# Performance work log

Hardware: AMD Instinct MI355X
Metric: run time of the kernel (lower is better)

Reference implementation:

```python
import jax, jax.numpy as jnp
import numpy as np

B, L, HID, H = 2, 384, 512, 8
D = HID // H  # head_dim = 64


def setup_inputs() -> dict:
    key = jax.random.key(0)
    ks = jax.random.split(key, 16)
    s = 0.02
    return {
        "query": jax.random.normal(ks[0], (B, L, HID), jnp.float32),
        "key_": jax.random.normal(ks[1], (B, L, HID), jnp.float32),
        "value": jax.random.normal(ks[2], (B, L, HID), jnp.float32),
        "mask": jnp.ones((B, 1, 1, L), jnp.int32),
        # fc_q/k/v/o: nn.Linear(hid_dim, hid_dim)
        "Wq": jax.random.normal(ks[3], (HID, HID), jnp.float32) * s,
        "bq": jnp.zeros((HID,), jnp.float32),
        "Wk": jax.random.normal(ks[4], (HID, HID), jnp.float32) * s,
        "bk": jnp.zeros((HID,), jnp.float32),
        "Wv": jax.random.normal(ks[5], (HID, HID), jnp.float32) * s,
        "bv": jnp.zeros((HID,), jnp.float32),
        "Wo": jax.random.normal(ks[6], (HID, HID), jnp.float32) * s,
        "bo": jnp.zeros((HID,), jnp.float32),
        # additive-attention score MLP: W1, W2: Linear(D, D); v: Linear(D, 1)
        "W1": jax.random.normal(ks[7], (D, D), jnp.float32) * s,
        "b1": jnp.zeros((D,), jnp.float32),
        "W2": jax.random.normal(ks[8], (D, D), jnp.float32) * s,
        "b2": jnp.zeros((D,), jnp.float32),
        "vw": jax.random.normal(ks[9], (1, D), jnp.float32) * s,
        "vb": jnp.zeros((1,), jnp.float32),
    }


def reference(query, key_, value, mask, Wq, bq, Wk, bk, Wv, bv, Wo, bo,
              W1, b1, W2, b2, vw, vb):
    b = query.shape[0]
    # projections (torch Linear: x @ W.T + b)
    Q = query @ Wq.T + bq
    K = key_ @ Wk.T + bk
    V = value @ Wv.T + bv
    # [b, h, l, d]
    def split_heads(x):
        return x.reshape(b, -1, H, D).transpose(0, 2, 1, 3)
    Q, K, V = split_heads(Q), split_heads(K), split_heads(V)
    # additive (Bahdanau-style) score: v^T tanh(W1 q + W2 k)
    tQ = Q @ W1.T + b1            # [b, h, lq, d]
    tK = K @ W2.T + b2            # [b, h, lk, d]
    e = jnp.tanh(tQ[:, :, :, None, :] + tK[:, :, None, :, :])  # [b,h,lq,lk,d]
    energy = jnp.einsum('bhqkd,d->bhqk', e, vw[0]) + vb[0]      # [b,h,lq,lk]
    energy = jnp.where(mask == 0, jnp.float32(-1e10), energy)
    attention = jax.nn.softmax(energy, axis=-1)
    x = jnp.einsum('bhqk,bhkd->bhqd', attention, V)  # dropout p=0 (eval)
    x = x.transpose(0, 2, 1, 3).reshape(b, -1, HID)
    x = x @ Wo.T + bo
    return x, attention
```

## Files before the change

kernel.cpp:

```cpp
#include <hip/hip_runtime.h>

#define BATCH 2
#define LSEQ 384
#define NHID 512
#define NH 8
#define DH 64
#define BH (BATCH*NH)
#define XELEMS ((size_t)768 * NHID)
#define TQ 8
#define QTILES (LSEQ/TQ)

typedef unsigned short ushort_t;
typedef __attribute__((ext_vector_type(8))) short bf16x8;
typedef __attribute__((ext_vector_type(4))) float f32x4;

__device__ __forceinline__ float bf2f(ushort_t u) {
    unsigned int v = ((unsigned int)u) << 16;
    return __uint_as_float(v);
}
__device__ __forceinline__ ushort_t f2bf(float f) {
    unsigned int u = __float_as_uint(f);
    unsigned int lsb = (u >> 16) & 1u;
    u += 0x7fffu + lsb;
    return (ushort_t)(u >> 16);
}
__device__ __forceinline__ float ld1(const void* p, size_t i, int f) {
    return f ? ((const float*)p)[i] : bf2f(((const ushort_t*)p)[i]);
}
__device__ __forceinline__ float4 ld4(const void* p, size_t i, int f) {
    if (f) return ((const float4*)p)[i >> 2];
    ushort4 u = ((const ushort4*)p)[i >> 2];
    return make_float4(bf2f(u.x), bf2f(u.y), bf2f(u.z), bf2f(u.w));
}
__device__ __forceinline__ int block_detect(const unsigned int* q, int* cnt) {
    int t = threadIdx.x;
    if (t == 0) *cnt = 0;
    __syncthreads();
    int n = blockDim.x < 256 ? blockDim.x : 256;
    if (t < n) {
        unsigned int elo = (q[t] >> 7) & 0xFFu;
        if (elo >= 100u && elo <= 150u) atomicAdd(cnt, 1);
    }
    __syncthreads();
    return (*cnt * 2 > n) ? 0 : 1;
}
__device__ __forceinline__ uint4 packu4(float4 a, float4 b) {
    uint4 r;
    r.x = (unsigned)f2bf(a.x) | ((unsigned)f2bf(a.y) << 16);
    r.y = (unsigned)f2bf(a.z) | ((unsigned)f2bf(a.w) << 16);
    r.z = (unsigned)f2bf(b.x) | ((unsigned)f2bf(b.y) << 16);
    r.w = (unsigned)f2bf(b.z) | ((unsigned)f2bf(b.w) << 16);
    return r;
}
__device__ __forceinline__ bf16x8 pack_bf8(float4 a, float4 b) {
    bf16x8 r;
    r[0] = (short)f2bf(a.x); r[1] = (short)f2bf(a.y);
    r[2] = (short)f2bf(a.z); r[3] = (short)f2bf(a.w);
    r[4] = (short)f2bf(b.x); r[5] = (short)f2bf(b.y);
    r[6] = (short)f2bf(b.z); r[7] = (short)f2bf(b.w);
    return r;
}

#define OFF_P     16
#define PSTRIDE   393216
#define OFF_BQE   2359312
#define OFF_BKE   2359824
#define OFF_ETQ   2360336
#define OFF_ETKT  2753552
#define OFF_VH    3146768
#define OFF_XH    3539984

#define LDSTR 72

__global__ __launch_bounds__(128) void gemm_qkv(
    const void* qp, const void* kp, const void* vp,
    const void* Wqp, const void* Wkp, const void* Wvp,
    const void* W1p, const void* W2p,
    const void* bqp, const void* bkp, const void* b1p, const void* b2p,
    float* __restrict__ ws)
{
    __shared__ int s_cnt;
    __shared__ ushort_t smA[32 * LDSTR];
    __shared__ ushort_t smB[64 * LDSTR];
    const int f = block_detect((const unsigned int*)qp, &s_cnt);

    const int z = blockIdx.z;
    const int mode = z >> 1, ks = z & 1;
    const int kbase = ks * 256;
    const void* A = (mode == 0) ? qp : (mode == 1) ? kp : vp;
    const void* W = (mode == 0) ? Wqp : (mode == 1) ? Wkp : Wvp;
    const void* W1x = (mode == 1) ? W2p : W1p;
    float* P = ws + OFF_P + (size_t)z * PSTRIDE;

    const int h    = blockIdx.x;
    const int col0 = h * 64;
    const int row0 = blockIdx.y * 32;
    const int t = threadIdx.x;
    const int w = t >> 6, l16 = t & 15, quad = (t & 63) >> 4;

    const int arow = t >> 2, acol = (t & 3) * 16;
    const int brow = t >> 1, bcol = (t & 1) * 32;
    const size_t abase = (size_t)(row0 + arow) * 512 + kbase + acol;
    const size_t bbase = (size_t)(col0 + brow) * 512 + kbase + bcol;

    float4 a4[4], b4[8];
    #pragma unroll
    for (int i = 0; i < 4; i++) a4[i] = ld4(A, abase + i * 4, f);
    #pragma unroll
    for (int i = 0; i < 8; i++) b4[i] = ld4(W, bbase + i * 4, f);

    f32x4 acc[4];
    #pragma unroll
    for (int nt = 0; nt < 4; nt++) acc[nt] = (f32x4){0.f, 0.f, 0.f, 0.f};

    for (int k0 = 0; k0 < 256; k0 += 64) {
        __syncthreads();
        *reinterpret_cast<uint4*>(&smA[arow * LDSTR + acol])     = packu4(a4[0], a4[1]);
        *reinterpret_cast<uint4*>(&smA[arow * LDSTR + acol + 8]) = packu4(a4[2], a4[3]);
        *reinterpret_cast<uint4*>(&smB[brow * LDSTR + bcol])      = packu4(b4[0], b4[1]);
        *reinterpret_cast<uint4*>(&smB[brow * LDSTR + bcol + 8])  = packu4(b4[2], b4[3]);
        *reinterpret_cast<uint4*>(&smB[brow * LDSTR + bcol + 16]) = packu4(b4[4], b4[5]);
        *reinterpret_cast<uint4*>(&smB[brow * LDSTR + bcol + 24]) = packu4(b4[6], b4[7]);
        __syncthreads();
        if (k0 + 64 < 256) {
            #pragma unroll
            for (int i = 0; i < 4; i++) a4[i] = ld4(A, abase + k0 + 64 + i * 4, f);
            #pragma unroll
            for (int i = 0; i < 8; i++) b4[i] = ld4(W, bbase + k0 + 64 + i * 4, f);
        }
        #pragma unroll
        for (int kk = 0; kk < 2; kk++) {
            bf16x8 af = *reinterpret_cast<const bf16x8*>(
                &smA[(w * 16 + l16) * LDSTR + kk * 32 + quad * 8]);
            #pragma unroll
            for (int nt = 0; nt < 4; nt++) {
                bf16x8 bfr = *reinterpret_cast<const bf16x8*>(
                    &smB[(nt * 16 + l16) * LDSTR + kk * 32 + quad * 8]);
                acc[nt] = __builtin_amdgcn_mfma_f32_16x16x32_bf16(af, bfr, acc[nt], 0, 0, 0);
            }
        }
    }

    if (mode == 2) {
        #pragma unroll
        for (int nt = 0; nt < 4; nt++) {
            int o = col0 + l16 + nt * 16;
            #pragma unroll
            for (int r = 0; r < 4; r++) {
                int m = row0 + w * 16 + quad * 4 + r;
                P[(size_t)m * 512 + o] = acc[nt][r];
            }
        }
    } else {
        #pragma unroll
        for (int nt = 0; nt < 4; nt++)
            #pragma unroll
            for (int r = 0; r < 4; r++)
                smA[(w * 16 + quad * 4 + r) * LDSTR + l16 + nt * 16] =
                    f2bf(acc[nt][r]);
        f32x4 acc2[4];
        #pragma unroll
        for (int nt = 0; nt < 4; nt++) acc2[nt] = (f32x4){0.f, 0.f, 0.f, 0.f};
        #pragma unroll
        for (int kk = 0; kk < 2; kk++) {
            bf16x8 af2 = *reinterpret_cast<const bf16x8*>(
                &smA[(w * 16 + l16) * LDSTR + kk * 32 + quad * 8]);
            #pragma unroll
            for (int nt = 0; nt < 4; nt++) {
                int od = nt * 16 + l16, j0 = kk * 32 + quad * 8;
                float4 wa = ld4(W1x, (size_t)od * 64 + j0, f);
                float4 wb = ld4(W1x, (size_t)od * 64 + j0 + 4, f);
                bf16x8 bfw = pack_bf8(wa, wb);
                acc2[nt] = __builtin_amdgcn_mfma_f32_16x16x32_bf16(af2, bfw, acc2[nt], 0, 0, 0);
            }
        }
        #pragma unroll
        for (int nt = 0; nt < 4; nt++) {
            int o = col0 + l16 + nt * 16;
            #pragma unroll
            for (int r = 0; r < 4; r++) {
                int m = row0 + w * 16 + quad * 4 + r;
                P[(size_t)m * 512 + o] = acc2[nt][r];
            }
        }
        if (blockIdx.y == 0 && ks == 0 && t < 64) {
            int od = t;
            const void* b1x = mode ? b2p : b1p;
            const void* bx  = mode ? bkp : bqp;
            float s = ld1(b1x, od, f);
            for (int j = 0; j < 64; j++)
                s = fmaf(ld1(W1x, (size_t)od * 64 + j, f), ld1(bx, h * 64 + j, f), s);
            ws[(mode ? OFF_BKE : OFF_BQE) + col0 + od] = s;
        }
    }
}

__global__ __launch_bounds__(256) void finalize(
    const void* qp, const void* bvp,
    const float* __restrict__ ws_in, float* __restrict__ ws)
{
    __shared__ int s_cnt;
    __shared__ __align__(16) float T[64 * 68];
    const int f = block_detect((const unsigned int*)qp, &s_cnt);
    const int blk = blockIdx.x;
    const int tid = threadIdx.x;

    if (blk < 384 || blk >= 480) {
        const int isV = (blk >= 480);
        const float* P0 = ws_in + OFF_P + (size_t)(isV ? 4 : 0) * PSTRIDE;
        const float* P1 = P0 + PSTRIDE;
        float* Out = ws + (isV ? OFF_VH : OFF_ETQ);
        int gid = (isV ? blk - 480 : blk) * 256 + tid;
        int m = gid >> 7;
        int o4 = (gid & 127) * 4;
        float4 p0 = *reinterpret_cast<const float4*>(P0 + (size_t)m * 512 + o4);
        float4 p1 = *reinterpret_cast<const float4*>(P1 + (size_t)m * 512 + o4);
        float4 bb;
        if (isV) bb = ld4(bvp, o4, f);
        else     bb = *reinterpret_cast<const float4*>(ws_in + OFF_BQE + o4);
        float4 r;
        if (isV) {
            r.x = p0.x + p1.x + bb.x; r.y = p0.y + p1.y + bb.y;
            r.z = p0.z + p1.z + bb.z; r.w = p0.w + p1.w + bb.w;
        } else {
            r.x = __expf(2.f * (p0.x + p1.x + bb.x));
            r.y = __expf(2.f * (p0.y + p1.y + bb.y));
            r.z = __expf(2.f * (p0.z + p1.z + bb.z));
            r.w = __expf(2.f * (p0.w + p1.w + bb.w));
        }
        int b = m / LSEQ, l = m % LSEQ, h = o4 >> 6, d = o4 & 63;
        *reinterpret_cast<float4*>(&Out[(size_t)((b * NH + h) * LSEQ + l) * 64 + d]) = r;
    } else {
        int blk2 = blk - 384;
        int bh = blk2 / 6, l0 = (blk2 % 6) * 64;
        int b = bh >> 3, h = bh & 7;
        const float* P0 = ws_in + OFF_P + (size_t)2 * PSTRIDE;
        const float* P1 = P0 + PSTRIDE;
        #pragma unroll
        for (int it = 0; it < 4; it++) {
            int li = (tid >> 4) + it * 16;
            int d4 = (tid & 15) * 4;
            size_t src = (size_t)(b * LSEQ + l0 + li) * 512 + h * 64 + d4;
            float4 p0 = *reinterpret_cast<const float4*>(P0 + src);
            float4 p1 = *reinterpret_cast<const float4*>(P1 + src);
            const float4 bb = *reinterpret_cast<const float4*>(ws_in + OFF_BKE + h * 64 + d4);
            T[(d4 + 0) * 68 + li] = __expf(2.f * (p0.x + p1.x + bb.x));
            T[(d4 + 1) * 68 + li] = __expf(2.f * (p0.y + p1.y + bb.y));
            T[(d4 + 2) * 68 + li] = __expf(2.f * (p0.z + p1.z + bb.z));
            T[(d4 + 3) * 68 + li] = __expf(2.f * (p0.w + p1.w + bb.w));
        }
        __syncthreads();
        float* Out = ws + OFF_ETKT;
        #pragma unroll
        for (int it = 0; it < 4; it++) {
            int d = (tid >> 4) + it * 16;
            int l4 = (tid & 15) * 4;
            float4 v = *reinterpret_cast<const float4*>(&T[d * 68 + l4]);
            *reinterpret_cast<float4*>(&Out[(size_t)(bh * 64 + d) * LSEQ + l0 + l4]) = v;
        }
    }
}

__global__ __launch_bounds__(384, 6) void attn_kernel(
    const void* qp, const void* vwp, const void* vbp,
    const float* __restrict__ ws_in, float* __restrict__ ws,
    const int* __restrict__ mask, void* __restrict__ dout)
{
    __shared__ int s_cnt;
    const int f = block_detect((const unsigned int*)qp, &s_cnt);

    const float* Etq = ws_in + OFF_ETQ;
    const float* Etk = ws_in + OFF_ETKT;
    const float* Vh  = ws_in + OFF_VH;
    float* Xh = ws + OFF_XH;

    const int bid = blockIdx.x;
    const int qt = bid % QTILES;
    const int bh = bid / QTILES;
    const int q0 = qt * TQ;
    const int b  = bh >> 3;
    const int h  = bh & 7;
    const int t  = threadIdx.x;
    const int wave = t >> 6;

    __shared__ __align__(16) float etq8[64][TQ];
    __shared__ float vws[64];
    __shared__ float ps[TQ][LSEQ];
    __shared__ float red[6][TQ][16][4];
    __shared__ float rsum[TQ][6];
    __shared__ float s_vb;

    for (int i = t; i < TQ * 64; i += 384) {
        int qi = i >> 6, d = i & 63;
        etq8[d][qi] = Etq[(size_t)(bh * LSEQ + q0 + qi) * 64 + d];
    }
    if (t < 64) {
        float v = ld1(vwp, t, f);
        vws[t] = v;
        #pragma unroll
        for (int off = 32; off > 0; off >>= 1) v += __shfl_xor(v, off, 64);
        if (t == 0) s_vb = ld1(vbp, 0, f) + v;
    }
    const int mok = mask[b * LSEQ + t];
    __syncthreads();
    const float vbSum = s_vb;

    float e2[TQ] = {0.f, 0.f, 0.f, 0.f, 0.f, 0.f, 0.f, 0.f};
    const float* ekp = Etk + (size_t)bh * 64 * LSEQ + t;
    #pragma unroll 4
    for (int d = 0; d < 64; d++) {
        float ekv = ekp[(size_t)d * LSEQ];
        float4 eqA = *reinterpret_cast<const float4*>(&etq8[d][0]);
        float4 eqB = *reinterpret_cast<const float4*>(&etq8[d][4]);
        float wv = vws[d];
        e2[0] = fmaf(wv, __builtin_amdgcn_rcpf(fmaf(eqA.x, ekv, 1.0f)), e2[0]);
        e2[1] = fmaf(wv, __builtin_amdgcn_rcpf(fmaf(eqA.y, ekv, 1.0f)), e2[1]);
        e2[2] = fmaf(wv, __builtin_amdgcn_rcpf(fmaf(eqA.z, ekv, 1.0f)), e2[2]);
        e2[3] = fmaf(wv, __builtin_amdgcn_rcpf(fmaf(eqA.w, ekv, 1.0f)), e2[3]);
        e2[4] = fmaf(wv, __builtin_amdgcn_rcpf(fmaf(eqB.x, ekv, 1.0f)), e2[4]);
        e2[5] = fmaf(wv, __builtin_amdgcn_rcpf(fmaf(eqB.y, ekv, 1.0f)), e2[5]);
        e2[6] = fmaf(wv, __builtin_amdgcn_rcpf(fmaf(eqB.z, ekv, 1.0f)), e2[6]);
        e2[7] = fmaf(wv, __builtin_amdgcn_rcpf(fmaf(eqB.w, ekv, 1.0f)), e2[7]);
    }

    float p[TQ];
    #pragma unroll
    for (int qi = 0; qi < TQ; qi++) {
        float en = fmaf(-2.0f, e2[qi], vbSum);
        if (mok == 0) en = -1e10f;
        p[qi] = __expf(en);
        float s = p[qi];
        #pragma unroll
        for (int off = 32; off > 0; off >>= 1) s += __shfl_xor(s, off, 64);
        if ((t & 63) == 0) rsum[qi][wave] = s;
    }
    __syncthreads();
    #pragma unroll
    for (int qi = 0; qi < TQ; qi++) {
        float gs = rsum[qi][0] + rsum[qi][1] + rsum[qi][2] +
                   rsum[qi][3] + rsum[qi][4] + rsum[qi][5];
        p[qi] *= 1.0f / gs;
        ps[qi][t] = p[qi];
        size_t aidx = XELEMS + (size_t)(bh * LSEQ + q0 + qi) * LSEQ + t;
        if (f) ((float*)dout)[aidx] = p[qi];
        else   ((ushort_t*)dout)[aidx] = f2bf(p[qi]);
    }
    __syncthreads();

    const int dq = t & 15;
    const int ksub = t >> 4;
    const float* vb4 = Vh + (size_t)bh * LSEQ * 64 + dq * 4;
    float4 acc[TQ];
    #pragma unroll
    for (int qi = 0; qi < TQ; qi++) acc[qi] = make_float4(0.f, 0.f, 0.f, 0.f);
    for (int kk = ksub; kk < LSEQ; kk += 24) {
        float4 v4 = *reinterpret_cast<const float4*>(vb4 + (size_t)kk * 64);
        #pragma unroll
        for (int qi = 0; qi < TQ; qi++) {
            float pq = ps[qi][kk];
            acc[qi].x = fmaf(pq, v4.x, acc[qi].x);
            acc[qi].y = fmaf(pq, v4.y, acc[qi].y);
            acc[qi].z = fmaf(pq, v4.z, acc[qi].z);
            acc[qi].w = fmaf(pq, v4.w, acc[qi].w);
        }
    }
    #pragma unroll
    for (int qi = 0; qi < TQ; qi++) {
        #pragma unroll
        for (int off = 16; off <= 32; off <<= 1) {
            acc[qi].x += __shfl_xor(acc[qi].x, off, 64);
            acc[qi].y += __shfl_xor(acc[qi].y, off, 64);
            acc[qi].z += __shfl_xor(acc[qi].z, off, 64);
            acc[qi].w += __shfl_xor(acc[qi].w, off, 64);
        }
    }
    if ((t & 63) < 16) {
        #pragma unroll
        for (int qi = 0; qi < TQ; qi++) {
            red[wave][qi][dq][0] = acc[qi].x;
            red[wave][qi][dq][1] = acc[qi].y;
            red[wave][qi][dq][2] = acc[qi].z;
            red[wave][qi][dq][3] = acc[qi].w;
        }
    }
    __syncthreads();
    if (t < 256) {
        int d = t & 63;
        #pragma unroll
        for (int half = 0; half < 2; half++) {
            int qi = (t >> 6) + half * 4;
            float sx = 0.f;
            #pragma unroll
            for (int w = 0; w < 6; w++) sx += red[w][qi][d >> 2][d & 3];
            Xh[((size_t)(b * LSEQ + q0 + qi) * NH + h) * 64 + d] = sx;
        }
    }
}

__global__ __launch_bounds__(128) void gemm_out(
    const void* qp, const void* Wop,
    const float* __restrict__ ws_in, float* __restrict__ ws)
{
    __shared__ int s_cnt;
    __shared__ ushort_t smA[32 * LDSTR];
    __shared__ ushort_t smB[64 * LDSTR];
    const int f = block_detect((const unsigned int*)qp, &s_cnt);

    const float* Xh = ws_in + OFF_XH;
    const int ks = blockIdx.z;
    const int kbase = ks * 128;
    float* P = ws + OFF_P + (size_t)ks * PSTRIDE;

    const int col0 = blockIdx.x * 64;
    const int row0 = blockIdx.y * 32;
    const int t = threadIdx.x;
    const int w = t >> 6, l16 = t & 15, quad = (t & 63) >> 4;

    const int arow = t >> 2, acol = (t & 3) * 16;
    const int brow = t >> 1, bcol = (t & 1) * 32;
    const float* Ab = Xh + (size_t)(row0 + arow) * 512 + kbase + acol;
    const size_t bbase = (size_t)(col0 + brow) * 512 + kbase + bcol;

    float4 a4[4], b4[8];
    #pragma unroll
    for (int i = 0; i < 4; i++) a4[i] = *reinterpret_cast<const float4*>(Ab + i * 4);
    #pragma unroll
    for (int i = 0; i < 8; i++) b4[i] = ld4(Wop, bbase + i * 4, f);

    f32x4 acc[4];
    #pragma unroll
    for (int nt = 0; nt < 4; nt++) acc[nt] = (f32x4){0.f, 0.f, 0.f, 0.f};

    for (int k0 = 0; k0 < 128; k0 += 64) {
        __syncthreads();
        *reinterpret_cast<uint4*>(&smA[arow * LDSTR + acol])     = packu4(a4[0], a4[1]);
        *reinterpret_cast<uint4*>(&smA[arow * LDSTR + acol + 8]) = packu4(a4[2], a4[3]);
        *reinterpret_cast<uint4*>(&smB[brow * LDSTR + bcol])      = packu4(b4[0], b4[1]);
        *reinterpret_cast<uint4*>(&smB[brow * LDSTR + bcol + 8])  = packu4(b4[2], b4[3]);
        *reinterpret_cast<uint4*>(&smB[brow * LDSTR + bcol + 16]) = packu4(b4[4], b4[5]);
        *reinterpret_cast<uint4*>(&smB[brow * LDSTR + bcol + 24]) = packu4(b4[6], b4[7]);
        __syncthreads();
        if (k0 + 64 < 128) {
            #pragma unroll
            for (int i = 0; i < 4; i++)
                a4[i] = *reinterpret_cast<const float4*>(Ab + k0 + 64 + i * 4);
            #pragma unroll
            for (int i = 0; i < 8; i++) b4[i] = ld4(Wop, bbase + k0 + 64 + i * 4, f);
        }
        #pragma unroll
        for (int kk = 0; kk < 2; kk++) {
            bf16x8 af = *reinterpret_cast<const bf16x8*>(
                &smA[(w * 16 + l16) * LDSTR + kk * 32 + quad * 8]);
            #pragma unroll
            for (int nt = 0; nt < 4; nt++) {
                bf16x8 bfr = *reinterpret_cast<const bf16x8*>(
                    &smB[(nt * 16 + l16) * LDSTR + kk * 32 + quad * 8]);
                acc[nt] = __builtin_amdgcn_mfma_f32_16x16x32_bf16(af, bfr, acc[nt], 0, 0, 0);
            }
        }
    }

    #pragma unroll
    for (int nt = 0; nt < 4; nt++) {
        int n = col0 + l16 + nt * 16;
        #pragma unroll
        for (int r = 0; r < 4; r++) {
            int m = row0 + w * 16 + quad * 4 + r;
            P[(size_t)m * 512 + n] = acc[nt][r];
        }
    }
}

__global__ __launch_bounds__(256) void out_reduce(
    const void* qp, const void* bop,
    const float* __restrict__ ws_in, void* __restrict__ dout)
{
    __shared__ int s_cnt;
    const int f = block_detect((const unsigned int*)qp, &s_cnt);
    int gid = blockIdx.x * 256 + threadIdx.x;
    size_t idx = (size_t)gid * 4;
    int o4 = (int)(idx & 511);
    const float* P = ws_in + OFF_P;
    float4 s0 = *reinterpret_cast<const float4*>(P + idx);
    float4 s1 = *reinterpret_cast<const float4*>(P + PSTRIDE + idx);
    float4 s2 = *reinterpret_cast<const float4*>(P + 2 * (size_t)PSTRIDE + idx);
    float4 s3 = *reinterpret_cast<const float4*>(P + 3 * (size_t)PSTRIDE + idx);
    float4 bb = ld4(bop, o4, f);
    float4 r;
    r.x = (s0.x + s1.x) + (s2.x + s3.x) + bb.x;
    r.y = (s0.y + s1.y) + (s2.y + s3.y) + bb.y;
    r.z = (s0.z + s1.z) + (s2.z + s3.z) + bb.z;
    r.w = (s0.w + s1.w) + (s2.w + s3.w) + bb.w;
    if (f) {
        *reinterpret_cast<float4*>((float*)dout + idx) = r;
    } else {
        ushort4 u;
        u.x = f2bf(r.x); u.y = f2bf(r.y); u.z = f2bf(r.z); u.w = f2bf(r.w);
        *reinterpret_cast<ushort4*>((ushort_t*)dout + idx) = u;
    }
}

extern "C" void kernel_launch(void* const* d_in, const int* in_sizes, int n_in,
                              void* d_out, int out_size, void* d_ws, size_t ws_size,
                              hipStream_t stream)
{
    const void* qp = d_in[0];
    const void* kp = d_in[1];
    const void* vp = d_in[2];
    const int* mask = (const int*)d_in[3];
    const void* Wqp = d_in[4];  const void* bqp = d_in[5];
    const void* Wkp = d_in[6];  const void* bkp = d_in[7];
    const void* Wvp = d_in[8];  const void* bvp = d_in[9];
    const void* Wop = d_in[10]; const void* bop = d_in[11];
    const void* W1p = d_in[12]; const void* b1p = d_in[13];
    const void* W2p = d_in[14]; const void* b2p = d_in[15];
    const void* vwp = d_in[16]; const void* vbp = d_in[17];

    float* ws = (float*)d_ws;

    gemm_qkv<<<dim3(8, 24, 6), 128, 0, stream>>>(qp, kp, vp, Wqp, Wkp, Wvp,
                                                 W1p, W2p, bqp, bkp, b1p, b2p, ws);
    finalize<<<864, 256, 0, stream>>>(qp, bvp, ws, ws);
    attn_kernel<<<BH * QTILES, 384, 0, stream>>>(qp, vwp, vbp, ws, ws, mask, d_out);
    gemm_out<<<dim3(8, 24, 4), 128, 0, stream>>>(qp, Wop, ws, ws);
    out_reduce<<<384, 256, 0, stream>>>(qp, bop, ws, d_out);
}
```

Baseline: 168.0 us.

## Store K energy row-major and read it with float4 loads in attention

The exp(2·K) tensor is now written in the same [bh][l][d] layout as Q and V. This removes the LDS-transpose branch in finalize, and all three regions share one simple elementwise path over 1152 blocks. The attention kernel reads each thread's K row as 16 float4 loads instead of 64 strided scalar loads. The price is that a wave's K loads are now scattered across 64 rows rather than coalesced along l, so the kernel leans more on cache reuse. The bf16 packing helpers also switch to a byte-permute intrinsic.

```diff
diff --git a/kernel.cpp b/kernel.cpp
--- a/kernel.cpp
+++ b/kernel.cpp
@@ -24,6 +24,12 @@
     u += 0x7fffu + lsb;
     return (ushort_t)(u >> 16);
 }
+__device__ __forceinline__ unsigned pk_bf16(float a, float b) {
+    unsigned ua = __float_as_uint(a), ub = __float_as_uint(b);
+    ua += 0x7fffu + ((ua >> 16) & 1u);
+    ub += 0x7fffu + ((ub >> 16) & 1u);
+    return __builtin_amdgcn_perm(ub, ua, 0x07060302);
+}
 __device__ __forceinline__ float ld1(const void* p, size_t i, int f) {
     return f ? ((const float*)p)[i] : bf2f(((const ushort_t*)p)[i]);
 }
@@ -46,19 +52,14 @@
 }
 __device__ __forceinline__ uint4 packu4(float4 a, float4 b) {
     uint4 r;
-    r.x = (unsigned)f2bf(a.x) | ((unsigned)f2bf(a.y) << 16);
-    r.y = (unsigned)f2bf(a.z) | ((unsigned)f2bf(a.w) << 16);
-    r.z = (unsigned)f2bf(b.x) | ((unsigned)f2bf(b.y) << 16);
-    r.w = (unsigned)f2bf(b.z) | ((unsigned)f2bf(b.w) << 16);
+    r.x = pk_bf16(a.x, a.y); r.y = pk_bf16(a.z, a.w);
+    r.z = pk_bf16(b.x, b.y); r.w = pk_bf16(b.z, b.w);
     return r;
 }
 __device__ __forceinline__ bf16x8 pack_bf8(float4 a, float4 b) {
-    bf16x8 r;
-    r[0] = (short)f2bf(a.x); r[1] = (short)f2bf(a.y);
-    r[2] = (short)f2bf(a.z); r[3] = (short)f2bf(a.w);
-    r[4] = (short)f2bf(b.x); r[5] = (short)f2bf(b.y);
-    r[6] = (short)f2bf(b.z); r[7] = (short)f2bf(b.w);
-    return r;
+    union { uint4 u; bf16x8 v; } r;
+    r.u = packu4(a, b);
+    return r.v;
 }
 
 #define OFF_P     16
@@ -66,7 +67,7 @@
 #define OFF_BQE   2359312
 #define OFF_BKE   2359824
 #define OFF_ETQ   2360336
-#define OFF_ETKT  2753552
+#define OFF_ETK   2753552
 #define OFF_VH    3146768
 #define OFF_XH    3539984
 
@@ -200,65 +201,36 @@
     const float* __restrict__ ws_in, float* __restrict__ ws)
 {
     __shared__ int s_cnt;
-    __shared__ __align__(16) float T[64 * 68];
     const int f = block_detect((const unsigned int*)qp, &s_cnt);
     const int blk = blockIdx.x;
+    const int region = blk / 384;
     const int tid = threadIdx.x;
 
-    if (blk < 384 || blk >= 480) {
-        const int isV = (blk >= 480);
-        const float* P0 = ws_in + OFF_P + (size_t)(isV ? 4 : 0) * PSTRIDE;
-        const float* P1 = P0 + PSTRIDE;
-        float* Out = ws + (isV ? OFF_VH : OFF_ETQ);
-        int gid = (isV ? blk - 480 : blk) * 256 + tid;
-        int m = gid >> 7;
-        int o4 = (gid & 127) * 4;
-        float4 p0 = *reinterpret_cast<const float4*>(P0 + (size_t)m * 512 + o4);
-        float4 p1 = *reinterpret_cast<const float4*>(P1 + (size_t)m * 512 + o4);
-        float4 bb;
-        if (isV) bb = ld4(bvp, o4, f);
-        else     bb = *reinterpret_cast<const float4*>(ws_in + OFF_BQE + o4);
-        float4 r;
-        if (isV) {
-            r.x = p0.x + p1.x + bb.x; r.y = p0.y + p1.y + bb.y;
-            r.z = p0.z + p1.z + bb.z; r.w = p0.w + p1.w + bb.w;
-        } else {
-            r.x = __expf(2.f * (p0.x + p1.x + bb.x));
-            r.y = __expf(2.f * (p0.y + p1.y + bb.y));
-            r.z = __expf(2.f * (p0.z + p1.z + bb.z));
-            r.w = __expf(2.f * (p0.w + p1.w + bb.w));
-        }
-        int b = m / LSEQ, l = m % LSEQ, h = o4 >> 6, d = o4 & 63;
-        *reinterpret_cast<float4*>(&Out[(size_t)((b * NH + h) * LSEQ + l) * 64 + d]) = r;
+    const float* P0 = ws_in + OFF_P + (size_t)(region * 2) * PSTRIDE;
+    const float* P1 = P0 + PSTRIDE;
+    float* Out = ws + (region == 0 ? OFF_ETQ : region == 1 ? OFF_ETK : OFF_VH);
+
+    int gid = (blk % 384) * 256 + tid;
+    int m = gid >> 7;
+    int o4 = (gid & 127) * 4;
+    float4 p0 = *reinterpret_cast<const float4*>(P0 + (size_t)m * 512 + o4);
+    float4 p1 = *reinterpret_cast<const float4*>(P1 + (size_t)m * 512 + o4);
+    float4 bb;
+    if (region == 0)      bb = *reinterpret_cast<const float4*>(ws_in + OFF_BQE + o4);
+    else if (region == 1) bb = *reinterpret_cast<const float4*>(ws_in + OFF_BKE + o4);
+    else                  bb = ld4(bvp, o4, f);
+    float4 r;
+    if (region < 2) {
+        r.x = __expf(2.f * (p0.x + p1.x + bb.x));
+        r.y = __expf(2.f * (p0.y + p1.y + bb.y));
+        r.z = __expf(2.f * (p0.z + p1.z + bb.z));
+        r.w = __expf(2.f * (p0.w + p1.w + bb.w));
     } else {
-        int blk2 = blk - 384;
-        int bh = blk2 / 6, l0 = (blk2 % 6) * 64;
-        int b = bh >> 3, h = bh & 7;
-        const float* P0 = ws_in + OFF_P + (size_t)2 * PSTRIDE;
-        const float* P1 = P0 + PSTRIDE;
-        #pragma unroll
-        for (int it = 0; it < 4; it++) {
-            int li = (tid >> 4) + it * 16;
-            int d4 = (tid & 15) * 4;
-            size_t src = (size_t)(b * LSEQ + l0 + li) * 512 + h * 64 + d4;
-            float4 p0 = *reinterpret_cast<const float4*>(P0 + src);
-            float4 p1 = *reinterpret_cast<const float4*>(P1 + src);
-            const float4 bb = *reinterpret_cast<const float4*>(ws_in + OFF_BKE + h * 64 + d4);
-            T[(d4 + 0) * 68 + li] = __expf(2.f * (p0.x + p1.x + bb.x));
-            T[(d4 + 1) * 68 + li] = __expf(2.f * (p0.y + p1.y + bb.y));
-            T[(d4 + 2) * 68 + li] = __expf(2.f * (p0.z + p1.z + bb.z));
-            T[(d4 + 3) * 68 + li] = __expf(2.f * (p0.w + p1.w + bb.w));
-        }
-        __syncthreads();
-        float* Out = ws + OFF_ETKT;
-        #pragma unroll
-        for (int it = 0; it < 4; it++) {
-            int d = (tid >> 4) + it * 16;
-            int l4 = (tid & 15) * 4;
-            float4 v = *reinterpret_cast<const float4*>(&T[d * 68 + l4]);
-            *reinterpret_cast<float4*>(&Out[(size_t)(bh * 64 + d) * LSEQ + l0 + l4]) = v;
-        }
-    }
+        r.x = p0.x + p1.x + bb.x; r.y = p0.y + p1.y + bb.y;
+        r.z = p0.z + p1.z + bb.z; r.w = p0.w + p1.w + bb.w;
+    }
+    int b = m / LSEQ, l = m % LSEQ, h = o4 >> 6, d = o4 & 63;
+    *reinterpret_cast<float4*>(&Out[(size_t)((b * NH + h) * LSEQ + l) * 64 + d]) = r;
 }
 
 __global__ __launch_bounds__(384, 6) void attn_kernel(
@@ -270,7 +242,7 @@
     const int f = block_detect((const unsigned int*)qp, &s_cnt);
 
     const float* Etq = ws_in + OFF_ETQ;
-    const float* Etk = ws_in + OFF_ETKT;
+    const float* Etk = ws_in + OFF_ETK;
     const float* Vh  = ws_in + OFF_VH;
     float* Xh = ws + OFF_XH;
 
@@ -306,21 +278,26 @@
     const float vbSum = s_vb;
 
     float e2[TQ] = {0.f, 0.f, 0.f, 0.f, 0.f, 0.f, 0.f, 0.f};
-    const float* ekp = Etk + (size_t)bh * 64 * LSEQ + t;
+    const float* ekrow = Etk + (size_t)(bh * LSEQ + t) * 64;
     #pragma unroll 4
-    for (int d = 0; d < 64; d++) {
-        float ekv = ekp[(size_t)d * LSEQ];
-        float4 eqA = *reinterpret_cast<const float4*>(&etq8[d][0]);
-        float4 eqB = *reinterpret_cast<const float4*>(&etq8[d][4]);
-        float wv = vws[d];
-        e2[0] = fmaf(wv, __builtin_amdgcn_rcpf(fmaf(eqA.x, ekv, 1.0f)), e2[0]);
-        e2[1] = fmaf(wv, __builtin_amdgcn_rcpf(fmaf(eqA.y, ekv, 1.0f)), e2[1]);
-        e2[2] = fmaf(wv, __builtin_amdgcn_rcpf(fmaf(eqA.z, ekv, 1.0f)), e2[2]);
-        e2[3] = fmaf(wv, __builtin_amdgcn_rcpf(fmaf(eqA.w, ekv, 1.0f)), e2[3]);
-        e2[4] = fmaf(wv, __builtin_amdgcn_rcpf(fmaf(eqB.x, ekv, 1.0f)), e2[4]);
-        e2[5] = fmaf(wv, __builtin_amdgcn_rcpf(fmaf(eqB.y, ekv, 1.0f)), e2[5]);
-        e2[6] = fmaf(wv, __builtin_amdgcn_rcpf(fmaf(eqB.z, ekv, 1.0f)), e2[6]);
-        e2[7] = fmaf(wv, __builtin_amdgcn_rcpf(fmaf(eqB.w, ekv, 1.0f)), e2[7]);
+    for (int dv = 0; dv < 16; dv++) {
+        float4 ek4 = *reinterpret_cast<const float4*>(ekrow + dv * 4);
+        #pragma unroll
+        for (int j = 0; j < 4; j++) {
+            int d = dv * 4 + j;
+            float ekv = (j == 0) ? ek4.x : (j == 1) ? ek4.y : (j == 2) ? ek4.z : ek4.w;
+            float4 eqA = *reinterpret_cast<const float4*>(&etq8[d][0]);
+            float4 eqB = *reinterpret_cast<const float4*>(&etq8[d][4]);
+            float wv = vws[d];
+            e2[0] = fmaf(wv, __builtin_amdgcn_rcpf(fmaf(eqA.x, ekv, 1.0f)), e2[0]);
+            e2[1] = fmaf(wv, __builtin_amdgcn_rcpf(fmaf(eqA.y, ekv, 1.0f)), e2[1]);
+            e2[2] = fmaf(wv, __builtin_amdgcn_rcpf(fmaf(eqA.z, ekv, 1.0f)), e2[2]);
+            e2[3] = fmaf(wv, __builtin_amdgcn_rcpf(fmaf(eqA.w, ekv, 1.0f)), e2[3]);
+            e2[4] = fmaf(wv, __builtin_amdgcn_rcpf(fmaf(eqB.x, ekv, 1.0f)), e2[4]);
+            e2[5] = fmaf(wv, __builtin_amdgcn_rcpf(fmaf(eqB.y, ekv, 1.0f)), e2[5]);
+            e2[6] = fmaf(wv, __builtin_amdgcn_rcpf(fmaf(eqB.z, ekv, 1.0f)), e2[6]);
+            e2[7] = fmaf(wv, __builtin_amdgcn_rcpf(fmaf(eqB.w, ekv, 1.0f)), e2[7]);
+        }
     }
 
     float p[TQ];
@@ -520,7 +497,7 @@
 
     gemm_qkv<<<dim3(8, 24, 6), 128, 0, stream>>>(qp, kp, vp, Wqp, Wkp, Wvp,
                                                  W1p, W2p, bqp, bkp, b1p, b2p, ws);
-    finalize<<<864, 256, 0, stream>>>(qp, bvp, ws, ws);
+    finalize<<<1152, 256, 0, stream>>>(qp, bvp, ws, ws);
     attn_kernel<<<BH * QTILES, 384, 0, stream>>>(qp, vwp, vbp, ws, ws, mask, d_out);
     gemm_out<<<dim3(8, 24, 4), 128, 0, stream>>>(qp, Wop, ws, ws);
     out_reduce<<<384, 256, 0, stream>>>(qp, bop, ws, d_out);
```

After: 166.8 us. Within noise of the previous version (-0.7%).
